# Optimization experiments

Measured on AMD Instinct MI355X. Metric: run time of the kernel, lower is better.

## Reference

```python
import jax, jax.numpy as jnp
import numpy as np

DIM = 1024
N_HEADS = 16
HEAD_DIM = DIM // N_HEADS  # 64
THETA = 10000.0
B, S = 4, 1024


def _rope_full_dim(x):
    """RoPE applied over the FULL last dim (head_dim == model dim), matching the
    original module which builds RotaryEmbeddings(head_dim=args.dim) and applies
    it to [B, S, dim] before splitting into heads. Positions start at 0."""
    Bx, Sx, D = x.shape
    freq = 1.0 / (THETA ** (jnp.arange(0, D, 2, dtype=jnp.float32) / D))  # [D/2]
    ang = jnp.arange(Sx, dtype=jnp.float32)[:, None] * freq[None, :]      # [S, D/2]
    cos, sin = jnp.cos(ang), jnp.sin(ang)
    xp = x.astype(jnp.float32).reshape(Bx, Sx, D // 2, 2)
    x0, x1 = xp[..., 0], xp[..., 1]
    rot = jnp.stack([x0 * cos - x1 * sin, x0 * sin + x1 * cos], axis=-1)
    return rot.reshape(Bx, Sx, D).astype(x.dtype)


def setup_inputs() -> dict:
    key = jax.random.key(0)
    ks = jax.random.split(key, 5)
    scale = 1.0 / np.sqrt(DIM)
    x = jax.random.normal(ks[0], (B, S, DIM), dtype=jnp.float32)
    Wq = jax.random.normal(ks[1], (DIM, DIM), dtype=jnp.float32) * scale
    Wk = jax.random.normal(ks[2], (DIM, DIM), dtype=jnp.float32) * scale
    Wv = jax.random.normal(ks[3], (DIM, DIM), dtype=jnp.float32) * scale
    Wo = jax.random.normal(ks[4], (DIM, DIM), dtype=jnp.float32) * scale
    bo = jnp.zeros((DIM,), dtype=jnp.float32)
    return {"x": x, "Wq": Wq, "Wk": Wk, "Wv": Wv, "Wo": Wo, "bo": bo, "start_pos": 0}


def reference(x, Wq, Wk, Wv, Wo, bo, start_pos):
    # start_pos == 0: the zero-initialized KV cache write+read is an identity
    # (keys == xk, values == xv over [:, :S]); n_rep == 1 so repeat_kv is a no-op.
    # NOTE: the original applies NO causal mask.
    Bx, Sx, _ = x.shape
    xq = _rope_full_dim(x @ Wq.T)  # [B, S, DIM] (weights stored torch-style [out,in])
    xk = _rope_full_dim(x @ Wk.T)
    xv = x @ Wv.T
    q = xq.reshape(Bx, Sx, N_HEADS, HEAD_DIM).transpose(0, 2, 1, 3)  # [B,H,S,D]
    k = xk.reshape(Bx, Sx, N_HEADS, HEAD_DIM).transpose(0, 2, 1, 3)
    v = xv.reshape(Bx, Sx, N_HEADS, HEAD_DIM).transpose(0, 2, 1, 3)
    scores = jnp.einsum("bhqd,bhkd->bhqk", q, k) / np.float32(np.sqrt(HEAD_DIM))
    attn = jax.nn.softmax(scores.astype(jnp.float32), axis=-1).astype(q.dtype)
    out = jnp.einsum("bhqk,bhkd->bhqd", attn, v)          # [B,H,S,D]
    out = out.transpose(0, 2, 1, 3).reshape(Bx, Sx, DIM)  # [B,S,DIM]
    return out @ Wo.T + bo
```

## Files before the change

kernel.cpp:

```cpp
#include <hip/hip_runtime.h>
#include <cstdint>
#include <cstddef>

typedef _Float16 f16;
typedef __attribute__((ext_vector_type(8))) _Float16 h8v;
typedef __attribute__((ext_vector_type(4))) _Float16 h4v;
typedef __attribute__((ext_vector_type(2))) _Float16 h2v;
typedef __attribute__((ext_vector_type(4))) float f4v;

#define DIM 1024
#define SEQ 1024
#define NH 16
#define HD 64

#if __has_builtin(__builtin_amdgcn_exp2f)
#define EXP2(x) __builtin_amdgcn_exp2f(x)
#else
#define EXP2(x) exp2f(x)
#endif
#if __has_builtin(__builtin_amdgcn_rcpf)
#define RCP(x) __builtin_amdgcn_rcpf(x)
#else
#define RCP(x) (1.0f / (x))
#endif

__device__ __forceinline__ void gld16(const void* g, void* l) {
  __builtin_amdgcn_global_load_lds(
      (const __attribute__((address_space(1))) void*)g,
      (__attribute__((address_space(3))) void*)l, 16, 0, 0);
}

__device__ __forceinline__ f4v mfma16(h8v a, h8v b, f4v c) {
  return __builtin_amdgcn_mfma_f32_16x16x32_f16(a, b, c, 0, 0, 0);
}
__device__ __forceinline__ f4v mfma16k16(h4v a, h4v b, f4v c) {
  return __builtin_amdgcn_mfma_f32_16x16x16f16(a, b, c, 0, 0, 0);
}

__device__ __forceinline__ h4v pk4(float a, float b, float c, float d) {
  h2v lo = __builtin_bit_cast(h2v, __builtin_amdgcn_cvt_pkrtz(a, b));
  h2v hi = __builtin_bit_cast(h2v, __builtin_amdgcn_cvt_pkrtz(c, d));
  return (h4v){lo[0], lo[1], hi[0], hi[1]};
}

__device__ __forceinline__ void cvt_store4(f16* dst, float4 v) {
  *(h4v*)dst = (h4v){(f16)v.x, (f16)v.y, (f16)v.z, (f16)v.w};
}

__global__ __launch_bounds__(256) void convert_kernel(
    const float* __restrict__ x,  const float* __restrict__ Wq,
    const float* __restrict__ Wk, const float* __restrict__ Wv,
    const float* __restrict__ Wo,
    f16* __restrict__ xh, f16* __restrict__ wqkv, f16* __restrict__ woh)
{
  int i = blockIdx.x * 256 + threadIdx.x;
  cvt_store4(xh + 4 * (size_t)i, ((const float4*)x)[i]);
  if (i < DIM * DIM / 4) {
    cvt_store4(wqkv + 4 * (size_t)i,               ((const float4*)Wq)[i]);
    cvt_store4(wqkv + DIM * DIM + 4 * (size_t)i,   ((const float4*)Wk)[i]);
    cvt_store4(wqkv + 2 * DIM * DIM + 4 * (size_t)i, ((const float4*)Wv)[i]);
    cvt_store4(woh + 4 * (size_t)i,                ((const float4*)Wo)[i]);
  }
}

__global__ __launch_bounds__(256) void qkv_gemm(
    const f16* __restrict__ A, const f16* __restrict__ W,
    f16* __restrict__ Qh, f16* __restrict__ Kh, f16* __restrict__ Vt)
{
  __shared__ f16 lA[2][4096];
  __shared__ f16 lB[2][4096];
  const int m0 = blockIdx.x * 128;
  const int n0 = blockIdx.y * 128;
  const int tid = threadIdx.x;
  const int w = tid >> 6, lane = tid & 63, quad = lane >> 4, l16 = lane & 15;
  const int wm = (w >> 1) * 64, wn = (w & 1) * 64;

  const int c0 = tid, c1 = 256 + tid;
  const int r0 = c0 >> 2, kc0 = (c0 & 3) ^ ((r0 >> 1) & 3);
  const int r1 = c1 >> 2, kc1 = (c1 & 3) ^ ((r1 >> 1) & 3);
  const f16* gA0 = A + (size_t)(m0 + r0) * DIM + kc0 * 8;
  const f16* gA1 = A + (size_t)(m0 + r1) * DIM + kc1 * 8;
  const f16* gB0 = W + (size_t)(n0 + r0) * DIM + kc0 * 8;
  const f16* gB1 = W + (size_t)(n0 + r1) * DIM + kc1 * 8;
  const int d0 = (c0 & ~63) * 8, d1 = (c1 & ~63) * 8;

  int pA[4], pB[4];
#pragma unroll
  for (int t = 0; t < 4; ++t) {
    int r = wm + t * 16 + l16;
    pA[t] = r * 4 + (quad ^ ((r >> 1) & 3));
    int rn = wn + t * 16 + l16;
    pB[t] = rn * 4 + (quad ^ ((rn >> 1) & 3));
  }

  f4v acc[4][4] = {};

#define QKV_PREF(KT, BUF)                  \
  {                                        \
    const int ko = (KT) * 32;              \
    gld16(gA0 + ko, &lA[BUF][d0]);         \
    gld16(gA1 + ko, &lA[BUF][d1]);         \
    gld16(gB0 + ko, &lB[BUF][d0]);         \
    gld16(gB1 + ko, &lB[BUF][d1]);         \
  }

#define QKV_COMP(BUF)                                                \
  {                                                                  \
    h8v af[4], bf[4];                                                \
    _Pragma("unroll")                                                \
    for (int t = 0; t < 4; ++t) af[t] = *(const h8v*)&lA[BUF][pA[t] * 8]; \
    _Pragma("unroll")                                                \
    for (int t = 0; t < 4; ++t) bf[t] = *(const h8v*)&lB[BUF][pB[t] * 8]; \
    _Pragma("unroll")                                                \
    for (int i = 0; i < 4; ++i)                                      \
      _Pragma("unroll")                                              \
      for (int j = 0; j < 4; ++j)                                    \
        acc[i][j] = mfma16(af[i], bf[j], acc[i][j]);                 \
  }

  QKV_PREF(0, 0);
  for (int kt = 0; kt < DIM / 32; kt += 2) {
    __syncthreads();
    QKV_PREF(kt + 1, 1);
    QKV_COMP(0);
    __syncthreads();
    if (kt + 2 < DIM / 32) QKV_PREF(kt + 2, 0);
    QKV_COMP(1);
  }
#undef QKV_PREF
#undef QKV_COMP

  if (n0 < 2 * DIM) {
    f16* dst = (n0 < DIM) ? Qh : Kh;
    const float osc = (n0 < DIM) ? 0.18033688f : 1.0f;
#pragma unroll
    for (int i = 0; i < 4; ++i) {
      const int mb = m0 + wm + i * 16 + quad * 4;
#pragma unroll
      for (int j = 0; j < 4; ++j) {
        const int n = n0 + wn + j * 16 + l16;
        const int d = n & (DIM - 1);
        const float fr = exp2f(-0.025952563f * (float)(d >> 1));
        const float sgn = (d & 1) ? 1.0f : -1.0f;
        const int hh = d >> 6, dd = d & 63;
#pragma unroll
        for (int r = 0; r < 4; ++r) {
          const int m = mb + r;
          const int s = m & (SEQ - 1), b = m >> 10;
          const float v = acc[i][j][r];
          const float pt = __shfl_xor(v, 1, 64);
          float sn, cs;
          __sincosf((float)s * fr, &sn, &cs);
          dst[((size_t)(b * NH + hh) * SEQ + s) * HD + dd] =
              (f16)((v * cs + sgn * pt * sn) * osc);
        }
      }
    }
  } else {
#pragma unroll
    for (int i = 0; i < 4; ++i) {
      const int mb = m0 + wm + i * 16 + quad * 4;
      const int b = mb >> 10;
      const int sp = ((mb & (SEQ - 1)) & ~63) + quad * 16 + i * 4;
#pragma unroll
      for (int j = 0; j < 4; ++j) {
        const int d = (n0 - 2 * DIM) + wn + j * 16 + l16;
        const int hh = d >> 6, dd = d & 63;
        h4v vv = {(f16)acc[i][j][0], (f16)acc[i][j][1],
                  (f16)acc[i][j][2], (f16)acc[i][j][3]};
        *(h4v*)&Vt[((size_t)(b * NH + hh) * HD + dd) * SEQ + sp] = vv;
      }
    }
  }
}

__global__ __launch_bounds__(256) void attn_kernel(
    const f16* __restrict__ Q, const f16* __restrict__ K,
    const f16* __restrict__ V, f16* __restrict__ O)
{
  __shared__ f16 LK[2][4096];
  __shared__ f16 LV[2][4096];
  const int tid = threadIdx.x;
  const int w = tid >> 6, lane = tid & 63, quad = lane >> 4, l16 = lane & 15;
  const int bid = blockIdx.x;
  const int qt = bid >> 6, bh = bid & 63;
  const f16* Qb = Q + (size_t)bh * SEQ * HD;
  const f16* Kg = K + (size_t)bh * SEQ * HD;
  const f16* Vg = V + (size_t)bh * HD * SEQ;
  const int q0 = qt * 128 + w * 16;

  const h8v bq0a = *(const h8v*)&Qb[(size_t)(q0 + l16) * HD + quad * 8];
  const h8v bq0b = *(const h8v*)&Qb[(size_t)(q0 + l16) * HD + quad * 8 + 32];
  const h8v bq1a = *(const h8v*)&Qb[(size_t)(q0 + 64 + l16) * HD + quad * 8];
  const h8v bq1b = *(const h8v*)&Qb[(size_t)(q0 + 64 + l16) * HD + quad * 8 + 32];

  const int c0 = tid, c1 = 256 + tid;
  const int r0 = c0 >> 3, kc0 = (c0 & 7) ^ (r0 & 7);
  const int r1 = c1 >> 3, kc1 = (c1 & 7) ^ (r1 & 7);
  const f16* gK0 = Kg + (size_t)r0 * HD + kc0 * 8;
  const f16* gK1 = Kg + (size_t)r1 * HD + kc1 * 8;
  const f16* gV0 = Vg + (size_t)r0 * SEQ + kc0 * 8;
  const f16* gV1 = Vg + (size_t)r1 * SEQ + kc1 * 8;
  const int dk0 = (c0 & ~63) * 8, dk1 = (c1 & ~63) * 8;

  int koff[4][2];
#pragma unroll
  for (int j = 0; j < 4; ++j) {
    int r = j * 16 + l16;
#pragma unroll
    for (int kk = 0; kk < 2; ++kk)
      koff[j][kk] = (r * 8 + ((quad + 4 * kk) ^ (r & 7))) * 8;
  }
  int voff2[2];
#pragma unroll
  for (int jp = 0; jp < 2; ++jp)
    voff2[jp] = l16 * 64 + ((quad * 2 + jp) ^ (l16 & 7)) * 8;

  const h4v vones = {(f16)1.f, (f16)1.f, (f16)1.f, (f16)1.f};
  f4v accL0 = {}, accL1 = {};
  f4v accO0[4] = {}, accO1[4] = {};

#define ATTN_PREF(TT, BUF)                       \
  {                                              \
    const size_t kb = (size_t)(TT) * 64;         \
    gld16(gK0 + kb * HD, &LK[BUF][dk0]);         \
    gld16(gK1 + kb * HD, &LK[BUF][dk1]);         \
    gld16(gV0 + kb, &LV[BUF][dk0]);              \
    gld16(gV1 + kb, &LV[BUF][dk1]);              \
  }

#define ATTN_TILE(BUF)                                                       \
  {                                                                          \
    h8v kf[4][2];                                                            \
    _Pragma("unroll")                                                        \
    for (int j = 0; j < 4; ++j) {                                            \
      kf[j][0] = *(const h8v*)&LK[BUF][koff[j][0]];                          \
      kf[j][1] = *(const h8v*)&LK[BUF][koff[j][1]];                          \
    }                                                                        \
    f4v sc0[4], sc1[4];                                                      \
    _Pragma("unroll")                                                        \
    for (int j = 0; j < 4; ++j) {                                            \
      f4v z0 = {-12.f, -12.f, -12.f, -12.f};          \
      z0 = mfma16(kf[j][0], bq0a, z0);                                       \
      z0 = mfma16(kf[j][1], bq0b, z0);                                       \
      sc0[j] = z0;                                                           \
      f4v z1 = {-12.f, -12.f, -12.f, -12.f};                                 \
      z1 = mfma16(kf[j][0], bq1a, z1);                                       \
      z1 = mfma16(kf[j][1], bq1b, z1);                                       \
      sc1[j] = z1;                                                           \
    }                                                                        \
    h4v pf0[4], pf1[4];                                                      \
    _Pragma("unroll")                                                        \
    for (int j = 0; j < 4; ++j) {                                            \
      pf0[j] = pk4(EXP2(sc0[j][0]), EXP2(sc0[j][1]),                         \
                   EXP2(sc0[j][2]), EXP2(sc0[j][3]));                        \
      pf1[j] = pk4(EXP2(sc1[j][0]), EXP2(sc1[j][1]),                         \
                   EXP2(sc1[j][2]), EXP2(sc1[j][3]));                        \
    }                                                                        \
    h4v ps0 = (pf0[0] + pf0[1]) + (pf0[2] + pf0[3]);                         \
    h4v ps1 = (pf1[0] + pf1[1]) + (pf1[2] + pf1[3]);                         \
    accL0 = mfma16k16(ps0, vones, accL0);                                    \
    accL1 = mfma16k16(ps1, vones, accL1);                                    \
    _Pragma("unroll")                                                        \
    for (int dt = 0; dt < 4; ++dt) {                                         \
      _Pragma("unroll")                                                      \
      for (int jp = 0; jp < 2; ++jp) {                                       \
        const h8v vv = *(const h8v*)&LV[BUF][voff2[jp] + dt * 1024];         \
        const h4v vlo = __builtin_shufflevector(vv, vv, 0, 1, 2, 3);         \
        const h4v vhi = __builtin_shufflevector(vv, vv, 4, 5, 6, 7);         \
        accO0[dt] = mfma16k16(pf0[2 * jp], vlo, accO0[dt]);                  \
        accO1[dt] = mfma16k16(pf1[2 * jp], vlo, accO1[dt]);                  \
        accO0[dt] = mfma16k16(pf0[2 * jp + 1], vhi, accO0[dt]);              \
        accO1[dt] = mfma16k16(pf1[2 * jp + 1], vhi, accO1[dt]);              \
      }                                                                      \
    }                                                                        \
  }

  ATTN_PREF(0, 0);
  for (int t = 0; t < SEQ / 64; t += 2) {
    __syncthreads();
    ATTN_PREF(t + 1, 1);
    ATTN_TILE(0);
    __syncthreads();
    if (t + 2 < SEQ / 64) ATTN_PREF(t + 2, 0);
    ATTN_TILE(1);
  }
#undef ATTN_PREF
#undef ATTN_TILE

  f4v inv0, inv1;
#pragma unroll
  for (int r = 0; r < 4; ++r) { inv0[r] = RCP(accL0[r]); inv1[r] = RCP(accL1[r]); }

  const int b = bh >> 4, hh = bh & 15;
#pragma unroll
  for (int dt = 0; dt < 4; ++dt) {
    const int d = dt * 16 + l16;
#pragma unroll
    for (int r = 0; r < 4; ++r) {
      const int s0 = q0 + quad * 4 + r;
      O[(size_t)(b * SEQ + s0) * DIM + hh * HD + d] =
          (f16)(accO0[dt][r] * inv0[r]);
      O[(size_t)(b * SEQ + s0 + 64) * DIM + hh * HD + d] =
          (f16)(accO1[dt][r] * inv1[r]);
    }
  }
}

__global__ __launch_bounds__(256) void out_gemm(
    const f16* __restrict__ A, const f16* __restrict__ W,
    const float* __restrict__ bias, float* __restrict__ out)
{
  __shared__ f16 lA[2][2048];
  __shared__ f16 lB[2][4096];
  const int m0 = blockIdx.x * 64;
  const int n0 = blockIdx.y * 128;
  const int tid = threadIdx.x;
  const int w = tid >> 6, lane = tid & 63, quad = lane >> 4, l16 = lane & 15;
  const int wm = (w >> 1) * 32, wn = (w & 1) * 64;

  const int c0 = tid, c1 = 256 + tid;
  const int rA = c0 >> 2, kcA = (c0 & 3) ^ ((rA >> 1) & 3);
  const int rB1 = c1 >> 2, kcB1 = (c1 & 3) ^ ((rB1 >> 1) & 3);
  const f16* gA  = A + (size_t)(m0 + rA) * DIM + kcA * 8;
  const f16* gB0 = W + (size_t)(n0 + rA) * DIM + kcA * 8;
  const f16* gB1 = W + (size_t)(n0 + rB1) * DIM + kcB1 * 8;
  const int dA = (c0 & ~63) * 8, dB1 = (c1 & ~63) * 8;

  int pA_[2], pB_[4];
#pragma unroll
  for (int t = 0; t < 2; ++t) {
    int r = wm + t * 16 + l16;
    pA_[t] = r * 4 + (quad ^ ((r >> 1) & 3));
  }
#pragma unroll
  for (int t = 0; t < 4; ++t) {
    int rn = wn + t * 16 + l16;
    pB_[t] = rn * 4 + (quad ^ ((rn >> 1) & 3));
  }

  f4v acc[2][4] = {};

#define OUT_PREF(KT, BUF)                  \
  {                                        \
    const int ko = (KT) * 32;              \
    gld16(gA + ko, &lA[BUF][dA]);          \
    gld16(gB0 + ko, &lB[BUF][dA]);         \
    gld16(gB1 + ko, &lB[BUF][dB1]);        \
  }

#define OUT_COMP(BUF)                                                 \
  {                                                                   \
    h8v af[2], bf[4];                                                 \
    _Pragma("unroll")                                                 \
    for (int t = 0; t < 2; ++t) af[t] = *(const h8v*)&lA[BUF][pA_[t] * 8]; \
    _Pragma("unroll")                                                 \
    for (int t = 0; t < 4; ++t) bf[t] = *(const h8v*)&lB[BUF][pB_[t] * 8]; \
    _Pragma("unroll")                                                 \
    for (int i = 0; i < 2; ++i)                                       \
      _Pragma("unroll")                                               \
      for (int j = 0; j < 4; ++j)                                     \
        acc[i][j] = mfma16(af[i], bf[j], acc[i][j]);                  \
  }

  OUT_PREF(0, 0);
  for (int kt = 0; kt < DIM / 32; kt += 2) {
    __syncthreads();
    OUT_PREF(kt + 1, 1);
    OUT_COMP(0);
    __syncthreads();
    if (kt + 2 < DIM / 32) OUT_PREF(kt + 2, 0);
    OUT_COMP(1);
  }
#undef OUT_PREF
#undef OUT_COMP

#pragma unroll
  for (int i = 0; i < 2; ++i) {
#pragma unroll
    for (int j = 0; j < 4; ++j) {
      const int n = n0 + wn + j * 16 + l16;
      const float bv = bias[n];
#pragma unroll
      for (int r = 0; r < 4; ++r) {
        const int m = m0 + wm + i * 16 + quad * 4 + r;
        out[(size_t)m * DIM + n] = acc[i][j][r] + bv;
      }
    }
  }
}

extern "C" void kernel_launch(void* const* d_in, const int* in_sizes, int n_in,
                              void* d_out, int out_size, void* d_ws, size_t ws_size,
                              hipStream_t stream)
{
  (void)in_sizes; (void)n_in; (void)out_size; (void)ws_size;
  const float* x  = (const float*)d_in[0];
  const float* Wq = (const float*)d_in[1];
  const float* Wk = (const float*)d_in[2];
  const float* Wv = (const float*)d_in[3];
  const float* Wo = (const float*)d_in[4];
  const float* bo = (const float*)d_in[5];
  float* out = (float*)d_out;

  char* ws = (char*)d_ws;
  const size_t MB = (size_t)1 << 20;
  f16* xh   = (f16*)(ws);
  f16* wqkv = (f16*)(ws + 8  * MB);
  f16* woh  = (f16*)(ws + 14 * MB);
  f16* Qh   = (f16*)(ws + 16 * MB);
  f16* Kh   = (f16*)(ws + 24 * MB);
  f16* Vt   = (f16*)(ws + 32 * MB);
  f16* Oh   = (f16*)(ws);

  convert_kernel<<<dim3(4096), 256, 0, stream>>>(x, Wq, Wk, Wv, Wo, xh, wqkv, woh);
  qkv_gemm<<<dim3(32, 24), 256, 0, stream>>>(xh, wqkv, Qh, Kh, Vt);
  attn_kernel<<<dim3(512), 256, 0, stream>>>(Qh, Kh, Vt, Oh);
  out_gemm<<<dim3(64, 8), 256, 0, stream>>>(Oh, woh, bo, out);
}
```

Before: 171.8 us.

## Load V fragments directly from global into registers and stage 128-key K tiles

The attention kernel no longer stages V through shared memory. Each lane reads its V fragments straight from global memory into registers, while K is staged in 128-key double-buffered tiles, so there are half as many block barriers per pass. The aim is to cut LDS traffic and synchronisation for V. In exchange it relies on global or L2 latency for the V reads, which are not prefetched far ahead, and adds register pressure from the 16 h8v V buffers.

```diff
diff --git a/kernel.cpp b/kernel.cpp
--- a/kernel.cpp
+++ b/kernel.cpp
@@ -178,8 +178,7 @@
     const f16* __restrict__ Q, const f16* __restrict__ K,
     const f16* __restrict__ V, f16* __restrict__ O)
 {
-  __shared__ f16 LK[2][4096];
-  __shared__ f16 LV[2][4096];
+  __shared__ f16 LK[2][8192];
   const int tid = threadIdx.x;
   const int w = tid >> 6, lane = tid & 63, quad = lane >> 4, l16 = lane & 15;
   const int bid = blockIdx.x;
@@ -194,14 +193,17 @@
   const h8v bq1a = *(const h8v*)&Qb[(size_t)(q0 + 64 + l16) * HD + quad * 8];
   const h8v bq1b = *(const h8v*)&Qb[(size_t)(q0 + 64 + l16) * HD + quad * 8 + 32];
 
-  const int c0 = tid, c1 = 256 + tid;
+  const int c0 = tid, c1 = 256 + tid, c2 = 512 + tid, c3 = 768 + tid;
   const int r0 = c0 >> 3, kc0 = (c0 & 7) ^ (r0 & 7);
   const int r1 = c1 >> 3, kc1 = (c1 & 7) ^ (r1 & 7);
+  const int r2 = c2 >> 3, kc2 = (c2 & 7) ^ (r2 & 7);
+  const int r3 = c3 >> 3, kc3 = (c3 & 7) ^ (r3 & 7);
   const f16* gK0 = Kg + (size_t)r0 * HD + kc0 * 8;
   const f16* gK1 = Kg + (size_t)r1 * HD + kc1 * 8;
-  const f16* gV0 = Vg + (size_t)r0 * SEQ + kc0 * 8;
-  const f16* gV1 = Vg + (size_t)r1 * SEQ + kc1 * 8;
+  const f16* gK2 = Kg + (size_t)r2 * HD + kc2 * 8;
+  const f16* gK3 = Kg + (size_t)r3 * HD + kc3 * 8;
   const int dk0 = (c0 & ~63) * 8, dk1 = (c1 & ~63) * 8;
+  const int dk2 = (c2 & ~63) * 8, dk3 = (c3 & ~63) * 8;
 
   int koff[4][2];
 #pragma unroll
@@ -211,31 +213,40 @@
     for (int kk = 0; kk < 2; ++kk)
       koff[j][kk] = (r * 8 + ((quad + 4 * kk) ^ (r & 7))) * 8;
   }
-  int voff2[2];
-#pragma unroll
-  for (int jp = 0; jp < 2; ++jp)
-    voff2[jp] = l16 * 64 + ((quad * 2 + jp) ^ (l16 & 7)) * 8;
+
+  const f16* Vf = Vg + (size_t)l16 * SEQ + quad * 16;
 
   const h4v vones = {(f16)1.f, (f16)1.f, (f16)1.f, (f16)1.f};
   f4v accL0 = {}, accL1 = {};
   f4v accO0[4] = {}, accO1[4] = {};
-
-#define ATTN_PREF(TT, BUF)                       \
-  {                                              \
-    const size_t kb = (size_t)(TT) * 64;         \
-    gld16(gK0 + kb * HD, &LK[BUF][dk0]);         \
-    gld16(gK1 + kb * HD, &LK[BUF][dk1]);         \
-    gld16(gV0 + kb, &LV[BUF][dk0]);              \
-    gld16(gV1 + kb, &LV[BUF][dk1]);              \
-  }
-
-#define ATTN_TILE(BUF)                                                       \
+  h8v vva[8], vvb[8];
+
+#define ATTN_PREF(TT, BUF)                            \
+  {                                                   \
+    const size_t kb = (size_t)(TT) * 128 * HD;        \
+    gld16(gK0 + kb, &LK[BUF][dk0]);                   \
+    gld16(gK1 + kb, &LK[BUF][dk1]);                   \
+    gld16(gK2 + kb, &LK[BUF][dk2]);                   \
+    gld16(gK3 + kb, &LK[BUF][dk3]);                   \
+  }
+
+#define ATTN_VLOAD(TT, H, VV)                                               \
+  {                                                                         \
+    _Pragma("unroll")                                                       \
+    for (int dt = 0; dt < 4; ++dt)                                          \
+      _Pragma("unroll")                                                     \
+      for (int jp = 0; jp < 2; ++jp)                                        \
+        VV[dt * 2 + jp] = *(const h8v*)&Vf[(size_t)(dt * 16) * SEQ +        \
+                                           (TT) * 128 + (H) * 64 + jp * 8]; \
+  }
+
+#define ATTN_COMP(BUF, H, VV)                                                \
   {                                                                          \
     h8v kf[4][2];                                                            \
     _Pragma("unroll")                                                        \
     for (int j = 0; j < 4; ++j) {                                            \
-      kf[j][0] = *(const h8v*)&LK[BUF][koff[j][0]];                          \
-      kf[j][1] = *(const h8v*)&LK[BUF][koff[j][1]];                          \
+      kf[j][0] = *(const h8v*)&LK[BUF][(H) * 4096 + koff[j][0]];             \
+      kf[j][1] = *(const h8v*)&LK[BUF][(H) * 4096 + koff[j][1]];             \
     }                                                                        \
     f4v sc0[4], sc1[4];                                                      \
     _Pragma("unroll")                                                        \
@@ -265,7 +276,7 @@
     for (int dt = 0; dt < 4; ++dt) {                                         \
       _Pragma("unroll")                                                      \
       for (int jp = 0; jp < 2; ++jp) {                                       \
-        const h8v vv = *(const h8v*)&LV[BUF][voff2[jp] + dt * 1024];         \
+        const h8v vv = VV[dt * 2 + jp];                                      \
         const h4v vlo = __builtin_shufflevector(vv, vv, 0, 1, 2, 3);         \
         const h4v vhi = __builtin_shufflevector(vv, vv, 4, 5, 6, 7);         \
         accO0[dt] = mfma16k16(pf0[2 * jp], vlo, accO0[dt]);                  \
@@ -277,16 +288,23 @@
   }
 
   ATTN_PREF(0, 0);
-  for (int t = 0; t < SEQ / 64; t += 2) {
-    __syncthreads();
+  for (int t = 0; t < 8; t += 2) {
+    __syncthreads();
+    ATTN_VLOAD(t, 0, vva);
     ATTN_PREF(t + 1, 1);
-    ATTN_TILE(0);
-    __syncthreads();
-    if (t + 2 < SEQ / 64) ATTN_PREF(t + 2, 0);
-    ATTN_TILE(1);
+    ATTN_COMP(0, 0, vva);
+    ATTN_VLOAD(t, 1, vvb);
+    ATTN_COMP(0, 1, vvb);
+    __syncthreads();
+    ATTN_VLOAD(t + 1, 0, vva);
+    if (t + 2 < 8) ATTN_PREF(t + 2, 0);
+    ATTN_COMP(1, 0, vva);
+    ATTN_VLOAD(t + 1, 1, vvb);
+    ATTN_COMP(1, 1, vvb);
   }
 #undef ATTN_PREF
-#undef ATTN_TILE
+#undef ATTN_VLOAD
+#undef ATTN_COMP
 
   f4v inv0, inv1;
 #pragma unroll
```

Measured after the change: 183.3 us. +6.7%, slower.

## Split attention query rows across eight waves instead of four

Applied to the files above, without the earlier changes.

The attention kernel now runs 512 threads per block, with each wave owning 16 query rows instead of two 16-row groups. Each thread issues one K and one V global-to-LDS load per tile instead of two. Per-wave register use (accumulators, score fragments) is roughly halved, which aims to raise occupancy and latency hiding. In exchange, K and V fragments read from LDS are reused across fewer rows, so LDS traffic per unit of MFMA work doubles, and block-wide syncs cover more waves.

```diff
diff --git a/kernel.cpp b/kernel.cpp
--- a/kernel.cpp
+++ b/kernel.cpp
@@ -174,7 +174,7 @@
   }
 }
 
-__global__ __launch_bounds__(256) void attn_kernel(
+__global__ __launch_bounds__(512) void attn_kernel(
     const f16* __restrict__ Q, const f16* __restrict__ K,
     const f16* __restrict__ V, f16* __restrict__ O)
 {
@@ -191,17 +191,12 @@
 
   const h8v bq0a = *(const h8v*)&Qb[(size_t)(q0 + l16) * HD + quad * 8];
   const h8v bq0b = *(const h8v*)&Qb[(size_t)(q0 + l16) * HD + quad * 8 + 32];
-  const h8v bq1a = *(const h8v*)&Qb[(size_t)(q0 + 64 + l16) * HD + quad * 8];
-  const h8v bq1b = *(const h8v*)&Qb[(size_t)(q0 + 64 + l16) * HD + quad * 8 + 32];
-
-  const int c0 = tid, c1 = 256 + tid;
+
+  const int c0 = tid;
   const int r0 = c0 >> 3, kc0 = (c0 & 7) ^ (r0 & 7);
-  const int r1 = c1 >> 3, kc1 = (c1 & 7) ^ (r1 & 7);
   const f16* gK0 = Kg + (size_t)r0 * HD + kc0 * 8;
-  const f16* gK1 = Kg + (size_t)r1 * HD + kc1 * 8;
   const f16* gV0 = Vg + (size_t)r0 * SEQ + kc0 * 8;
-  const f16* gV1 = Vg + (size_t)r1 * SEQ + kc1 * 8;
-  const int dk0 = (c0 & ~63) * 8, dk1 = (c1 & ~63) * 8;
+  const int dk0 = (c0 & ~63) * 8;
 
   int koff[4][2];
 #pragma unroll
@@ -217,16 +212,14 @@
     voff2[jp] = l16 * 64 + ((quad * 2 + jp) ^ (l16 & 7)) * 8;
 
   const h4v vones = {(f16)1.f, (f16)1.f, (f16)1.f, (f16)1.f};
-  f4v accL0 = {}, accL1 = {};
-  f4v accO0[4] = {}, accO1[4] = {};
+  f4v accL0 = {};
+  f4v accO0[4] = {};
 
 #define ATTN_PREF(TT, BUF)                       \
   {                                              \
     const size_t kb = (size_t)(TT) * 64;         \
     gld16(gK0 + kb * HD, &LK[BUF][dk0]);         \
-    gld16(gK1 + kb * HD, &LK[BUF][dk1]);         \
     gld16(gV0 + kb, &LV[BUF][dk0]);              \
-    gld16(gV1 + kb, &LV[BUF][dk1]);              \
   }
 
 #define ATTN_TILE(BUF)                                                       \
@@ -237,30 +230,22 @@
       kf[j][0] = *(const h8v*)&LK[BUF][koff[j][0]];                          \
       kf[j][1] = *(const h8v*)&LK[BUF][koff[j][1]];                          \
     }                                                                        \
-    f4v sc0[4], sc1[4];                                                      \
+    f4v sc0[4];                                                              \
     _Pragma("unroll")                                                        \
     for (int j = 0; j < 4; ++j) {                                            \
       f4v z0 = {-12.f, -12.f, -12.f, -12.f};          \
       z0 = mfma16(kf[j][0], bq0a, z0);                                       \
       z0 = mfma16(kf[j][1], bq0b, z0);                                       \
       sc0[j] = z0;                                                           \
-      f4v z1 = {-12.f, -12.f, -12.f, -12.f};                                 \
-      z1 = mfma16(kf[j][0], bq1a, z1);                                       \
-      z1 = mfma16(kf[j][1], bq1b, z1);                                       \
-      sc1[j] = z1;                                                           \
     }                                                                        \
-    h4v pf0[4], pf1[4];                                                      \
+    h4v pf0[4];                                                              \
     _Pragma("unroll")                                                        \
     for (int j = 0; j < 4; ++j) {                                            \
       pf0[j] = pk4(EXP2(sc0[j][0]), EXP2(sc0[j][1]),                         \
                    EXP2(sc0[j][2]), EXP2(sc0[j][3]));                        \
-      pf1[j] = pk4(EXP2(sc1[j][0]), EXP2(sc1[j][1]),                         \
-                   EXP2(sc1[j][2]), EXP2(sc1[j][3]));                        \
     }                                                                        \
     h4v ps0 = (pf0[0] + pf0[1]) + (pf0[2] + pf0[3]);                         \
-    h4v ps1 = (pf1[0] + pf1[1]) + (pf1[2] + pf1[3]);                         \
     accL0 = mfma16k16(ps0, vones, accL0);                                    \
-    accL1 = mfma16k16(ps1, vones, accL1);                                    \
     _Pragma("unroll")                                                        \
     for (int dt = 0; dt < 4; ++dt) {                                         \
       _Pragma("unroll")                                                      \
@@ -269,9 +254,7 @@
         const h4v vlo = __builtin_shufflevector(vv, vv, 0, 1, 2, 3);         \
         const h4v vhi = __builtin_shufflevector(vv, vv, 4, 5, 6, 7);         \
         accO0[dt] = mfma16k16(pf0[2 * jp], vlo, accO0[dt]);                  \
-        accO1[dt] = mfma16k16(pf1[2 * jp], vlo, accO1[dt]);                  \
         accO0[dt] = mfma16k16(pf0[2 * jp + 1], vhi, accO0[dt]);              \
-        accO1[dt] = mfma16k16(pf1[2 * jp + 1], vhi, accO1[dt]);              \
       }                                                                      \
     }                                                                        \
   }
@@ -288,9 +271,9 @@
 #undef ATTN_PREF
 #undef ATTN_TILE
 
-  f4v inv0, inv1;
-#pragma unroll
-  for (int r = 0; r < 4; ++r) { inv0[r] = RCP(accL0[r]); inv1[r] = RCP(accL1[r]); }
+  f4v inv0;
+#pragma unroll
+  for (int r = 0; r < 4; ++r) inv0[r] = RCP(accL0[r]);
 
   const int b = bh >> 4, hh = bh & 15;
 #pragma unroll
@@ -301,8 +284,6 @@
       const int s0 = q0 + quad * 4 + r;
       O[(size_t)(b * SEQ + s0) * DIM + hh * HD + d] =
           (f16)(accO0[dt][r] * inv0[r]);
-      O[(size_t)(b * SEQ + s0 + 64) * DIM + hh * HD + d] =
-          (f16)(accO1[dt][r] * inv1[r]);
     }
   }
 }
@@ -415,6 +396,6 @@
 
   convert_kernel<<<dim3(4096), 256, 0, stream>>>(x, Wq, Wk, Wv, Wo, xh, wqkv, woh);
   qkv_gemm<<<dim3(32, 24), 256, 0, stream>>>(xh, wqkv, Qh, Kh, Vt);
-  attn_kernel<<<dim3(512), 256, 0, stream>>>(Qh, Kh, Vt, Oh);
+  attn_kernel<<<dim3(512), 512, 0, stream>>>(Qh, Kh, Vt, Oh);
   out_gemm<<<dim3(64, 8), 256, 0, stream>>>(Oh, woh, bo, out);
 }
```

After: 172.6 us. Within noise of the previous version (+0.5%).

## Enlarge QKV GEMM tiles to 256x256 with triple-buffered LDS pipeline

Applied to the files above, without the earlier changes.

The QKV projection GEMM moves from 128x128 tiles with 256 threads to 256x256 tiles with 512 threads. It uses a three-stage LDS ring buffer with explicit vmcnt waits, interleaves global prefetch with MFMA groups, raises wave priority around the MFMAs, and swizzles the block index so neighbouring blocks share tiles. The aim is more reuse per loaded tile and better overlap of memory with compute. In exchange there are only 192 blocks on the many CUs of the MI355X (fewer than one wave of blocks across the device), higher register and LDS pressure, and hand-written barrier ordering that is fragile.

```diff
diff --git a/kernel.cpp b/kernel.cpp
--- a/kernel.cpp
+++ b/kernel.cpp
@@ -46,6 +46,13 @@
 __device__ __forceinline__ void cvt_store4(f16* dst, float4 v) {
   *(h4v*)dst = (h4v){(f16)v.x, (f16)v.y, (f16)v.z, (f16)v.w};
 }
+
+#define BARRIER_FENCED                                    \
+  {                                                       \
+    asm volatile("" ::: "memory");                        \
+    __builtin_amdgcn_s_barrier();                         \
+    asm volatile("" ::: "memory");                        \
+  }
 
 __global__ __launch_bounds__(256) void convert_kernel(
     const float* __restrict__ x,  const float* __restrict__ Wq,
@@ -63,19 +70,22 @@
   }
 }
 
-__global__ __launch_bounds__(256) void qkv_gemm(
+__global__ __launch_bounds__(512, 1) void qkv_gemm(
     const f16* __restrict__ A, const f16* __restrict__ W,
     f16* __restrict__ Qh, f16* __restrict__ Kh, f16* __restrict__ Vt)
 {
-  __shared__ f16 lA[2][4096];
-  __shared__ f16 lB[2][4096];
-  const int m0 = blockIdx.x * 128;
-  const int n0 = blockIdx.y * 128;
+  __shared__ __align__(16) f16 lA[3][8192];
+  __shared__ __align__(16) f16 lB[3][8192];
+  const int id = blockIdx.x;
+  const int swz = (id & 7) * 24 + (id >> 3);
+  const int m0 = (swz / 12) * 256;
+  const int n0 = (swz % 12) * 256;
   const int tid = threadIdx.x;
   const int w = tid >> 6, lane = tid & 63, quad = lane >> 4, l16 = lane & 15;
-  const int wm = (w >> 1) * 64, wn = (w & 1) * 64;
-
-  const int c0 = tid, c1 = 256 + tid;
+  const int wm = (w >> 2) * 128, wn = (w & 3) * 64;
+  (void)lane;
+
+  const int c0 = tid, c1 = 512 + tid;
   const int r0 = c0 >> 2, kc0 = (c0 & 3) ^ ((r0 >> 1) & 3);
   const int r1 = c1 >> 2, kc1 = (c1 & 3) ^ ((r1 >> 1) & 3);
   const f16* gA0 = A + (size_t)(m0 + r0) * DIM + kc0 * 8;
@@ -84,57 +94,75 @@
   const f16* gB1 = W + (size_t)(n0 + r1) * DIM + kc1 * 8;
   const int d0 = (c0 & ~63) * 8, d1 = (c1 & ~63) * 8;
 
-  int pA[4], pB[4];
-#pragma unroll
-  for (int t = 0; t < 4; ++t) {
+  int pA[8], pB[4];
+#pragma unroll
+  for (int t = 0; t < 8; ++t) {
     int r = wm + t * 16 + l16;
     pA[t] = r * 4 + (quad ^ ((r >> 1) & 3));
+  }
+#pragma unroll
+  for (int t = 0; t < 4; ++t) {
     int rn = wn + t * 16 + l16;
     pB[t] = rn * 4 + (quad ^ ((rn >> 1) & 3));
   }
 
-  f4v acc[4][4] = {};
-
-#define QKV_PREF(KT, BUF)                  \
-  {                                        \
-    const int ko = (KT) * 32;              \
-    gld16(gA0 + ko, &lA[BUF][d0]);         \
-    gld16(gA1 + ko, &lA[BUF][d1]);         \
-    gld16(gB0 + ko, &lB[BUF][d0]);         \
-    gld16(gB1 + ko, &lB[BUF][d1]);         \
-  }
-
-#define QKV_COMP(BUF)                                                \
-  {                                                                  \
-    h8v af[4], bf[4];                                                \
-    _Pragma("unroll")                                                \
-    for (int t = 0; t < 4; ++t) af[t] = *(const h8v*)&lA[BUF][pA[t] * 8]; \
-    _Pragma("unroll")                                                \
-    for (int t = 0; t < 4; ++t) bf[t] = *(const h8v*)&lB[BUF][pB[t] * 8]; \
-    _Pragma("unroll")                                                \
-    for (int i = 0; i < 4; ++i)                                      \
-      _Pragma("unroll")                                              \
-      for (int j = 0; j < 4; ++j)                                    \
-        acc[i][j] = mfma16(af[i], bf[j], acc[i][j]);                 \
-  }
-
-  QKV_PREF(0, 0);
-  for (int kt = 0; kt < DIM / 32; kt += 2) {
-    __syncthreads();
-    QKV_PREF(kt + 1, 1);
-    QKV_COMP(0);
-    __syncthreads();
-    if (kt + 2 < DIM / 32) QKV_PREF(kt + 2, 0);
-    QKV_COMP(1);
-  }
-#undef QKV_PREF
-#undef QKV_COMP
+  f4v acc[8][4] = {};
+
+  gld16(gA0, &lA[0][d0]); gld16(gB0, &lB[0][d0]);
+  gld16(gA1, &lA[0][d1]); gld16(gB1, &lB[0][d1]);
+  gld16(gA0 + 32, &lA[1][d0]); gld16(gB0 + 32, &lB[1][d0]);
+  gld16(gA1 + 32, &lA[1][d1]); gld16(gB1 + 32, &lB[1][d1]);
+  asm volatile("s_waitcnt vmcnt(4)" ::: "memory");
+  __builtin_amdgcn_s_barrier();
+  asm volatile("" ::: "memory");
+
+  int cur = 0, sb = 2;
+  for (int t = 0; t < 32; ++t) {
+    const f16* __restrict__ cA = &lA[cur][0];
+    const f16* __restrict__ cB = &lB[cur][0];
+    const int ko = (t + 2) * 32;
+    const bool st = t < 30;
+    h8v af[8], bf[4];
+
+#pragma unroll
+    for (int i = 0; i < 4; ++i) af[i] = *(const h8v*)&cA[pA[i] * 8];
+#pragma unroll
+    for (int j = 0; j < 4; ++j) bf[j] = *(const h8v*)&cB[pB[j] * 8];
+    if (st) { gld16(gA0 + ko, &lA[sb][d0]); gld16(gB0 + ko, &lB[sb][d0]); }
+    BARRIER_FENCED;
+    __builtin_amdgcn_s_setprio(1);
+#pragma unroll
+    for (int i = 0; i < 4; ++i)
+#pragma unroll
+      for (int j = 0; j < 4; ++j)
+        acc[i][j] = mfma16(af[i], bf[j], acc[i][j]);
+    __builtin_amdgcn_s_setprio(0);
+    BARRIER_FENCED;
+
+#pragma unroll
+    for (int i = 4; i < 8; ++i) af[i] = *(const h8v*)&cA[pA[i] * 8];
+    if (st) { gld16(gA1 + ko, &lA[sb][d1]); gld16(gB1 + ko, &lB[sb][d1]); }
+    BARRIER_FENCED;
+    __builtin_amdgcn_s_setprio(1);
+#pragma unroll
+    for (int i = 4; i < 8; ++i)
+#pragma unroll
+      for (int j = 0; j < 4; ++j)
+        acc[i][j] = mfma16(af[i], bf[j], acc[i][j]);
+    __builtin_amdgcn_s_setprio(0);
+    if (t <= 29)      asm volatile("s_waitcnt vmcnt(4)" ::: "memory");
+    else if (t == 30) asm volatile("s_waitcnt vmcnt(0)" ::: "memory");
+    BARRIER_FENCED;
+
+    cur = (cur == 2) ? 0 : cur + 1;
+    sb  = (sb  == 2) ? 0 : sb  + 1;
+  }
 
   if (n0 < 2 * DIM) {
     f16* dst = (n0 < DIM) ? Qh : Kh;
     const float osc = (n0 < DIM) ? 0.18033688f : 1.0f;
 #pragma unroll
-    for (int i = 0; i < 4; ++i) {
+    for (int i = 0; i < 8; ++i) {
       const int mb = m0 + wm + i * 16 + quad * 4;
 #pragma unroll
       for (int j = 0; j < 4; ++j) {
@@ -158,10 +186,10 @@
     }
   } else {
 #pragma unroll
-    for (int i = 0; i < 4; ++i) {
+    for (int i = 0; i < 8; ++i) {
       const int mb = m0 + wm + i * 16 + quad * 4;
       const int b = mb >> 10;
-      const int sp = ((mb & (SEQ - 1)) & ~63) + quad * 16 + i * 4;
+      const int sp = ((mb & (SEQ - 1)) & ~63) + quad * 16 + (i & 3) * 4;
 #pragma unroll
       for (int j = 0; j < 4; ++j) {
         const int d = (n0 - 2 * DIM) + wn + j * 16 + l16;
@@ -414,7 +442,7 @@
   f16* Oh   = (f16*)(ws);
 
   convert_kernel<<<dim3(4096), 256, 0, stream>>>(x, Wq, Wk, Wv, Wo, xh, wqkv, woh);
-  qkv_gemm<<<dim3(32, 24), 256, 0, stream>>>(xh, wqkv, Qh, Kh, Vt);
+  qkv_gemm<<<dim3(192), 512, 0, stream>>>(xh, wqkv, Qh, Kh, Vt);
   attn_kernel<<<dim3(512), 256, 0, stream>>>(Qh, Kh, Vt, Oh);
   out_gemm<<<dim3(64, 8), 256, 0, stream>>>(Oh, woh, bo, out);
 }
```

Measured after the change: 173.4 us. About the same (+1.0%).
